# Performance work log

Hardware: AMD Instinct MI355X
Metric: run time of the kernel (lower is better)

Reference implementation:

```python
import jax, jax.numpy as jnp
import numpy as np

B, N, CS, CZ, H, CH, G, P = 2, 384, 384, 128, 8, 16, 2, 8
CZ4 = CZ // 4
INF = 1e5
UMAX = 3.0     # self.u_max
LMAX = 2.0     # self.log_scale_max
SQRT_CH = CH ** 0.5


def quat_to_rot(q):
    q = q / jnp.linalg.norm(q, axis=-1, keepdims=True)
    w, x, y, z = q[..., 0], q[..., 1], q[..., 2], q[..., 3]
    R = jnp.stack([
        1 - 2 * (y * y + z * z), 2 * (x * y - w * z), 2 * (x * z + w * y),
        2 * (x * y + w * z), 1 - 2 * (x * x + z * z), 2 * (y * z - w * x),
        2 * (x * z - w * y), 2 * (y * z + w * x), 1 - 2 * (x * x + y * y)], axis=-1)
    return R.reshape(q.shape[:-1] + (3, 3))


def robust_nll(delta, sigma):
    # inline robust 3x3 Cholesky solve: dist_sq = d^T S^-1 d, log_det = ln|S|
    eps = 1e-8
    s00 = sigma[..., 0, 0]; s01 = sigma[..., 0, 1]; s02 = sigma[..., 0, 2]
    s11 = sigma[..., 1, 1]; s12 = sigma[..., 1, 2]; s22 = sigma[..., 2, 2]
    d0 = delta[..., 0]; d1 = delta[..., 1]; d2 = delta[..., 2]
    l00_sq = jnp.maximum(s00, eps); inv_l00 = jax.lax.rsqrt(l00_sq)
    l10 = s01 * inv_l00; l20 = s02 * inv_l00
    l11_sq = jnp.maximum(s11 - l10 * l10, eps); inv_l11 = jax.lax.rsqrt(l11_sq)
    l21 = (s12 - l20 * l10) * inv_l11
    l22_sq = jnp.maximum(s22 - l20 * l20 - l21 * l21, eps); inv_l22 = jax.lax.rsqrt(l22_sq)
    log_det = jnp.log(l00_sq) + jnp.log(l11_sq) + jnp.log(l22_sq)
    y0 = d0 * inv_l00
    y1 = (d1 - l10 * y0) * inv_l11
    y2 = (d2 - l20 * y0 - l21 * y1) * inv_l22
    return y0 * y0 + y1 * y1 + y2 * y2, log_det


def iga_forward(s, z, mask, rot, trans, local_mean, scaling_log,
                Wq, Wk, Wv, Wb, bb, Wdz, bdz, Wqg, bqg, Wkg, bkg,
                Wvp, bvp, geo_scale, geo_bias, Wout, bout):
    # scalar q/k/v: [B,H,N,CH]
    q = (s @ Wq).reshape(B, N, H, CH).transpose(0, 2, 1, 3)
    k = (s @ Wk).reshape(B, N, H, CH).transpose(0, 2, 1, 3)
    v = (s @ Wv).reshape(B, N, H, CH).transpose(0, 2, 1, 3)
    logits = jnp.einsum('bhid,bhjd->bhij', q, k) / SQRT_CH
    # pair bias: [B,H,N,N]
    logits = logits + (z @ Wb + bb).transpose(0, 3, 1, 2)

    def parse(feat):  # -> u [B,N,H,G,3], s_log_delta [B,N,H,G,3]
        raw = feat.reshape(B, N, H, G, 6)
        return jnp.tanh(raw[..., :3]) * UMAX, jnp.tanh(raw[..., 3:]) * LMAX

    def to_global(u, sld):
        anchor = local_mean[:, :, None, None, :]
        base = scaling_log[:, :, None, None, :]
        sig_loc = jnp.maximum(jnp.exp(base + sld), 1e-6)
        pos = anchor + u * sig_loc
        mu = jnp.einsum('bnij,bnhgj->bnhgi', rot, pos) + trans[:, :, None, None, :]
        var = jnp.exp(2.0 * (base + sld))
        Sig = jnp.einsum('bnij,bnhgj,bnkj->bnhgik', rot, var, rot)  # R diag(var) R^T
        return mu.transpose(0, 2, 1, 3, 4), Sig.transpose(0, 2, 1, 3, 4, 5)

    qu, qs = parse(s @ Wqg + bqg)
    ku, ks = parse(s @ Wkg + bkg)
    q_mu, q_sig = to_global(qu, qs)   # [B,H,N,G,3], [B,H,N,G,3,3]
    k_mu, k_sig = to_global(ku, ks)
    delta = q_mu[:, :, :, None] - k_mu[:, :, None, :]      # [B,H,N,N,G,3]
    ssum = q_sig[:, :, :, None] + k_sig[:, :, None, :]     # [B,H,N,N,G,3,3]
    dist_sq, log_det = robust_nll(delta, ssum)
    geo = (-0.5 * dist_sq - 0.5 * log_det).sum(-1)          # [B,H,N,N]

    mask2d = mask[:, None, :, None] * mask[:, None, None, :]  # [B,1,N,N]
    a = jax.nn.softplus(geo_scale)[None, :, None, None]
    G_geo = a * (geo * mask2d) + geo_bias[None, :, None, None]
    logits = logits + G_geo + (1.0 - mask2d) * (-INF)
    w = jax.nn.softmax(logits, axis=-1)                      # [B,H,N,N]

    # scalar output
    o = jnp.einsum('bhij,bhjd->bihd', w, v).reshape(B, N, H * CH)
    # point output (IPA-style): to global, attend, back to local frame
    vpts = (s @ Wvp + bvp).reshape(B, N, H, P, 3)
    vpg = jnp.einsum('bnij,bnhpj->bnhpi', rot, vpts) + trans[:, :, None, None, :]
    vpg = vpg.transpose(0, 2, 1, 3, 4)                       # [B,H,N,P,3]
    opt = jnp.einsum('bhij,bhjpc->bhipc', w, vpg)            # [B,H,N,P,3]
    opt_local = jnp.einsum('bnji,bhnpj->bnhpi', rot, opt - trans[:, None, :, None, :])
    onorm = jnp.sqrt((opt_local ** 2).sum(-1) + 1e-8)        # [B,N,H,P]
    # pair output
    pz = z @ Wdz + bdz                                       # [B,N,N,CZ4]
    opair = jnp.einsum('bhij,bijc->bihc', w, pz)             # [B,N,H,CZ4]

    cat = jnp.concatenate([o, opt_local.reshape(B, N, H * P * 3),
                           onorm.reshape(B, N, H * P),
                           opair.reshape(B, N, H * CZ4)], axis=-1)  # [B,N,640]
    return cat @ Wout + bout


def setup_inputs() -> dict:
    ks = jax.random.split(jax.random.key(0), 24)
    rnd = lambda i, shape, sc=1.0: jax.random.normal(ks[i], shape, dtype=jnp.float32) * sc
    w = 0.02
    return dict(
        s=rnd(0, (B, N, CS)), z=rnd(1, (B, N, N, CZ)),
        mask=jnp.ones((B, N), jnp.float32),
        rot=quat_to_rot(rnd(2, (B, N, 4))),
        trans=rnd(3, (B, N, 3), 1.0),
        local_mean=rnd(4, (B, N, 3), 0.5),
        scaling_log=rnd(5, (B, N, 3), 0.1),
        Wq=rnd(6, (CS, H * CH), w), Wk=rnd(7, (CS, H * CH), w), Wv=rnd(8, (CS, H * CH), w),
        Wb=rnd(9, (CZ, H), w), bb=rnd(10, (H,), w),
        Wdz=rnd(11, (CZ, CZ4), w), bdz=rnd(12, (CZ4,), w),
        Wqg=rnd(13, (CS, H * G * 6), w), bqg=rnd(14, (H * G * 6,), w),
        Wkg=rnd(15, (CS, H * G * 6), w), bkg=rnd(16, (H * G * 6,), w),
        Wvp=rnd(17, (CS, H * P * 3), w), bvp=rnd(18, (H * P * 3,), w),
        geo_scale=jnp.ones((H,), jnp.float32), geo_bias=jnp.zeros((H,), jnp.float32),
        Wout=rnd(19, (H * (CH + P * 4 + CZ4), CS), w), bout=jnp.zeros((CS,), jnp.float32))


def reference(s, z, mask, rot, trans, local_mean, scaling_log, Wq, Wk, Wv, Wb, bb,
              Wdz, bdz, Wqg, bqg, Wkg, bkg, Wvp, bvp, geo_scale, geo_bias, Wout, bout):
    return iga_forward(s, z, mask, rot, trans, local_mean, scaling_log, Wq, Wk, Wv,
                       Wb, bb, Wdz, bdz, Wqg, bqg, Wkg, bkg, Wvp, bvp,
                       geo_scale, geo_bias, Wout, bout)
```

## Files before the change

kernel.cpp:

```cpp
#include <hip/hip_runtime.h>
#include <hip/hip_fp16.h>

#define NB   2
#define NN   384
#define NCS  384
#define NCZ  128
#define NH   8
#define NCH  16
#define NG   2
#define NP   8
#define NCZ4 32
#define BN   (NB*NN)
#define LINW 768

typedef _Float16 f16x8 __attribute__((ext_vector_type(8)));
typedef float    f32x4 __attribute__((ext_vector_type(4)));

__global__ void k_wprep(const float* __restrict__ Wb, const float* __restrict__ Wdz,
                        _Float16* __restrict__ wf) {
    int t = threadIdx.x;
    for (int e = t; e < 12*64*8; e += 256) {
        int r = e & 7, lane = (e >> 3) & 63, nk = e >> 9;
        int n = nk >> 2, kk = nk & 3;
        int c = kk*32 + (lane >> 4)*8 + r;
        int col = n*16 + (lane & 15);
        float w;
        if      (col < 8)  w = Wb[c*NH + col];
        else if (col < 40) w = Wdz[c*NCZ4 + (col-8)];
        else               w = 0.f;
        wf[e] = (_Float16)w;
    }
}

__global__ void k_rowlin(const float* __restrict__ s,
                         const float* __restrict__ Wq, const float* __restrict__ Wk,
                         const float* __restrict__ Wv,
                         const float* __restrict__ Wqg, const float* __restrict__ bqg,
                         const float* __restrict__ Wkg, const float* __restrict__ bkg,
                         const float* __restrict__ Wvp, const float* __restrict__ bvp,
                         float* __restrict__ lin,
                         float* __restrict__ kT, float* __restrict__ vT) {
    __shared__ float sl[4][NCS];
    int t  = threadIdx.x;
    int r0 = blockIdx.x * 4;
    for (int idx = t; idx < 4*NCS; idx += 256)
        sl[idx / NCS][idx % NCS] = s[(size_t)(r0 + idx/NCS)*NCS + (idx % NCS)];
    __syncthreads();
    int col = blockIdx.y * 256 + t;
    const float* W; int sw; float bias = 0.f;
    if      (col < 128) { W = Wq  + col;        sw = 128; }
    else if (col < 256) { W = Wk  + (col-128);  sw = 128; }
    else if (col < 384) { W = Wv  + (col-256);  sw = 128; }
    else if (col < 480) { W = Wqg + (col-384);  sw = 96;  bias = bqg[col-384]; }
    else if (col < 576) { W = Wkg + (col-480);  sw = 96;  bias = bkg[col-480]; }
    else                { W = Wvp + (col-576);  sw = 192; bias = bvp[col-576]; }
    float a0=0.f, a1=0.f, a2=0.f, a3=0.f;
    for (int c = 0; c < NCS; ++c) {
        float w = W[(size_t)c*sw];
        a0 = fmaf(sl[0][c], w, a0);
        a1 = fmaf(sl[1][c], w, a1);
        a2 = fmaf(sl[2][c], w, a2);
        a3 = fmaf(sl[3][c], w, a3);
    }
    lin[(size_t)(r0+0)*LINW + col] = a0 + bias;
    lin[(size_t)(r0+1)*LINW + col] = a1 + bias;
    lin[(size_t)(r0+2)*LINW + col] = a2 + bias;
    lin[(size_t)(r0+3)*LINW + col] = a3 + bias;
    if (col >= 128 && col < 384) {
        f32x4 v4; v4[0]=a0; v4[1]=a1; v4[2]=a2; v4[3]=a3;
        float* dst = (col < 256) ? (kT + (size_t)(col-128)*BN + r0)
                                 : (vT + (size_t)(col-256)*BN + r0);
        *(f32x4*)dst = v4;
    }
}

__global__ void k_geom(const float* __restrict__ lin, const float* __restrict__ rot,
                       const float* __restrict__ trans, const float* __restrict__ lm,
                       const float* __restrict__ sc,
                       float* __restrict__ qmu, float* __restrict__ qsig,
                       float* __restrict__ kmuT, float* __restrict__ ksigT,
                       float* __restrict__ vpgT) {
    int bn = blockIdx.x, t = threadIdx.x;
    __shared__ float R[9], T[3], A[3], Bs[3];
    if (t < 9) R[t] = rot[bn*9 + t];
    if (t < 3) { T[t] = trans[bn*3+t]; A[t] = lm[bn*3+t]; Bs[t] = sc[bn*3+t]; }
    __syncthreads();
    {
        int h = t >> 3, p = t & 7;
        const float* vr = lin + (size_t)bn*LINW + 576 + h*24 + p*3;
        float x = vr[0], y = vr[1], z = vr[2];
        int e = h*24 + p*3;
        vpgT[(size_t)(e+0)*BN + bn] = R[0]*x + R[1]*y + R[2]*z + T[0];
        vpgT[(size_t)(e+1)*BN + bn] = R[3]*x + R[4]*y + R[5]*z + T[1];
        vpgT[(size_t)(e+2)*BN + bn] = R[6]*x + R[7]*y + R[8]*z + T[2];
    }
    if (t < 32) {
        int side = t >> 4, item = t & 15;
        const float* raw = lin + (size_t)bn*LINW + (side ? 480 : 384) + item*6;
        float u0 = tanhf(raw[0])*3.f, u1 = tanhf(raw[1])*3.f, u2 = tanhf(raw[2])*3.f;
        float e0 = Bs[0] + tanhf(raw[3])*2.f;
        float e1 = Bs[1] + tanhf(raw[4])*2.f;
        float e2 = Bs[2] + tanhf(raw[5])*2.f;
        float sl0 = fmaxf(expf(e0), 1e-6f);
        float sl1 = fmaxf(expf(e1), 1e-6f);
        float sl2 = fmaxf(expf(e2), 1e-6f);
        float p0 = A[0] + u0*sl0, p1 = A[1] + u1*sl1, p2 = A[2] + u2*sl2;
        float mu0 = R[0]*p0 + R[1]*p1 + R[2]*p2 + T[0];
        float mu1 = R[3]*p0 + R[4]*p1 + R[5]*p2 + T[1];
        float mu2 = R[6]*p0 + R[7]*p1 + R[8]*p2 + T[2];
        float v0 = expf(2.f*e0), v1 = expf(2.f*e1), v2 = expf(2.f*e2);
        float s00 = R[0]*R[0]*v0 + R[1]*R[1]*v1 + R[2]*R[2]*v2;
        float s01 = R[0]*R[3]*v0 + R[1]*R[4]*v1 + R[2]*R[5]*v2;
        float s02 = R[0]*R[6]*v0 + R[1]*R[7]*v1 + R[2]*R[8]*v2;
        float s11 = R[3]*R[3]*v0 + R[4]*R[4]*v1 + R[5]*R[5]*v2;
        float s12 = R[3]*R[6]*v0 + R[4]*R[7]*v1 + R[5]*R[8]*v2;
        float s22 = R[6]*R[6]*v0 + R[7]*R[7]*v1 + R[8]*R[8]*v2;
        if (side) {
            kmuT[(size_t)(item*3+0)*BN + bn] = mu0;
            kmuT[(size_t)(item*3+1)*BN + bn] = mu1;
            kmuT[(size_t)(item*3+2)*BN + bn] = mu2;
            ksigT[(size_t)(item*6+0)*BN + bn] = s00;
            ksigT[(size_t)(item*6+1)*BN + bn] = s01;
            ksigT[(size_t)(item*6+2)*BN + bn] = s02;
            ksigT[(size_t)(item*6+3)*BN + bn] = s11;
            ksigT[(size_t)(item*6+4)*BN + bn] = s12;
            ksigT[(size_t)(item*6+5)*BN + bn] = s22;
        } else {
            float* mud = qmu + (size_t)bn*48 + item*3;
            mud[0]=mu0; mud[1]=mu1; mud[2]=mu2;
            float* sgd = qsig + (size_t)bn*96 + item*6;
            sgd[0]=s00; sgd[1]=s01; sgd[2]=s02; sgd[3]=s11; sgd[4]=s12; sgd[5]=s22;
        }
    }
}

__global__ void __launch_bounds__(256, 2)
k_attn(const float* __restrict__ z, const float* __restrict__ mask,
       const float* __restrict__ rot, const float* __restrict__ trans,
       const float* __restrict__ lin,
       const float* __restrict__ qmu, const float* __restrict__ qsig,
       const float* __restrict__ kmuT, const float* __restrict__ ksigT,
       const float* __restrict__ kT, const float* __restrict__ vT,
       const float* __restrict__ vpgT, const _Float16* __restrict__ wf,
       const float* __restrict__ bb, const float* __restrict__ bdz,
       const float* __restrict__ gsc, const float* __restrict__ gbi,
       float* __restrict__ cat) {
    __shared__ __align__(16) _Float16 zh[64*128];
    __shared__ float  logits[NH][NN];
    __shared__ __half pzl[NN][34];
    __shared__ float  qrow[128];
    __shared__ float  qmu_s[48], qsig_s[96];
    __shared__ float  Rm[9], Tv[3];
    __shared__ float  aH[NH], bH[NH];
    __shared__ float  bias_s[48];
    __shared__ float  maskI;

    int t  = threadIdx.x;
    int lane = t & 63, w = t >> 6;
    int b  = blockIdx.x / NN, i = blockIdx.x % NN;
    int bi = b*NN + i;
    const float* zbase = z + (size_t)bi*NN*NCZ;
    const size_t boff = (size_t)b*NN;

    const float* zrow0 = zbase + (size_t)(t >> 5)*NCZ + (t & 31)*4;
    float4 preA[8], preB[8];
    #pragma unroll
    for (int p = 0; p < 8; ++p) preA[p] = *(const float4*)(zrow0 + (size_t)(p*8)*NCZ);
    #pragma unroll
    for (int p = 0; p < 8; ++p) preB[p] = *(const float4*)(zrow0 + (size_t)(64 + p*8)*NCZ);

    if (t < 128) qrow[t] = lin[(size_t)bi*LINW + t];
    if (t < 48)  qmu_s[t] = qmu[(size_t)bi*48 + t];
    if (t < 48)  bias_s[t] = (t < 8) ? bb[t] : ((t < 40) ? bdz[t-8] : 0.f);
    if (t >= 64 && t < 160) qsig_s[t-64] = qsig[(size_t)bi*96 + (t-64)];
    if (t >= 160 && t < 169) Rm[t-160] = rot[bi*9 + (t-160)];
    if (t >= 169 && t < 172) Tv[t-169] = trans[bi*3 + (t-169)];
    if (t >= 176 && t < 184) {
        int h = t-176;
        float x = gsc[h];
        aH[h] = (x > 20.f) ? x : log1pf(expf(x));
        bH[h] = gbi[h];
    }
    if (t == 255) maskI = mask[bi];
    __syncthreads();

    {
        int h = t >> 5, lnn = t & 31;
        float qv[16];
        #pragma unroll
        for (int d = 0; d < 16; ++d) qv[d] = qrow[h*16 + d];
        float qm[6], qs[12];
        #pragma unroll
        for (int e = 0; e < 6; ++e)  qm[e] = qmu_s[h*6 + e];
        #pragma unroll
        for (int e = 0; e < 12; ++e) qs[e] = qsig_s[h*12 + e];
        float ascale = aH[h], hbias = bH[h], mI = maskI;
        #pragma unroll 1
        for (int jj = 0; jj < 3; ++jj) {
            int j4 = jj*128 + lnn*4;
            const float* kp = kT + (size_t)(h*16)*BN + boff + j4;
            f32x4 qk = {0.f,0.f,0.f,0.f};
            #pragma unroll
            for (int d = 0; d < 16; ++d) {
                f32x4 kv = *(const f32x4*)(kp + (size_t)d*BN);
                #pragma unroll
                for (int r = 0; r < 4; ++r) qk[r] = fmaf(qv[d], kv[r], qk[r]);
            }
            f32x4 geo = {0.f,0.f,0.f,0.f};
            #pragma unroll
            for (int g = 0; g < NG; ++g) {
                const float* kmb = kmuT + (size_t)((h*2+g)*3)*BN + boff + j4;
                f32x4 km0 = *(const f32x4*)(kmb);
                f32x4 km1 = *(const f32x4*)(kmb + BN);
                f32x4 km2 = *(const f32x4*)(kmb + 2*BN);
                const float* ksb = ksigT + (size_t)((h*2+g)*6)*BN + boff + j4;
                f32x4 ks0 = *(const f32x4*)(ksb);
                f32x4 ks1 = *(const f32x4*)(ksb + BN);
                f32x4 ks2 = *(const f32x4*)(ksb + 2*BN);
                f32x4 ks3 = *(const f32x4*)(ksb + 3*BN);
                f32x4 ks4 = *(const f32x4*)(ksb + 4*BN);
                f32x4 ks5 = *(const f32x4*)(ksb + 5*BN);
                #pragma unroll
                for (int r = 0; r < 4; ++r) {
                    float d0 = qm[g*3+0] - km0[r];
                    float d1 = qm[g*3+1] - km1[r];
                    float d2 = qm[g*3+2] - km2[r];
                    float s00 = qs[g*6+0] + ks0[r];
                    float s01 = qs[g*6+1] + ks1[r];
                    float s02 = qs[g*6+2] + ks2[r];
                    float s11 = qs[g*6+3] + ks3[r];
                    float s12 = qs[g*6+4] + ks4[r];
                    float s22 = qs[g*6+5] + ks5[r];
                    float l00 = fmaxf(s00, 1e-8f);
                    float i00 = rsqrtf(l00);
                    float l10 = s01*i00, l20 = s02*i00;
                    float l11 = fmaxf(s11 - l10*l10, 1e-8f);
                    float i11 = rsqrtf(l11);
                    float l21 = (s12 - l20*l10)*i11;
                    float l22 = fmaxf(s22 - l20*l20 - l21*l21, 1e-8f);
                    float i22 = rsqrtf(l22);
                    float ld = __logf(l00) + __logf(l11) + __logf(l22);
                    float y0 = d0*i00;
                    float y1 = (d1 - l10*y0)*i11;
                    float y2 = (d2 - l20*y0 - l21*y1)*i22;
                    geo[r] += -0.5f*(y0*y0 + y1*y1 + y2*y2 + ld);
                }
            }
            f32x4 mv = *(const f32x4*)(mask + boff + j4);
            f32x4 lg;
            #pragma unroll
            for (int r = 0; r < 4; ++r) {
                float m2 = mI * mv[r];
                lg[r] = qk[r]*0.25f + ascale*(geo[r]*m2) + hbias + (1.f - m2)*(-100000.f);
            }
            *(f32x4*)&logits[h][j4] = lg;
        }
    }

    f16x8 bfr[12];
    #pragma unroll
    for (int nk = 0; nk < 12; ++nk)
        bfr[nk] = ((const f16x8*)wf)[nk*64 + lane];

    int srow0 = t >> 5;
    int scb   = (t & 31) * 8;
    int sswz  = (srow0 & 7) << 4;
    int arow  = w*16 + (lane & 15);
    int abase = arow*256 + ((lane >> 4) << 4);
    int akey  = (lane & 7) << 4;
    int ccol  = lane & 15;
    int cjl   = w*16 + (lane >> 4)*4;

#define CHUNK_BODY(CH, PRE)                                                          \
    {                                                                                \
        _Pragma("unroll")                                                            \
        for (int p = 0; p < 8; ++p) {                                                \
            union { _Float16 h[4]; unsigned long long u; } pk;                       \
            pk.h[0] = (_Float16)PRE[p].x; pk.h[1] = (_Float16)PRE[p].y;              \
            pk.h[2] = (_Float16)PRE[p].z; pk.h[3] = (_Float16)PRE[p].w;              \
            *(unsigned long long*)((char*)zh + (p*8 + srow0)*256 + (scb ^ sswz)) = pk.u; \
        }                                                                            \
        if ((CH) + 2 < 6) {                                                          \
            const float* src = zbase + (size_t)((CH+2)*64)*NCZ + (size_t)(t>>5)*NCZ  \
                               + (t & 31)*4;                                         \
            _Pragma("unroll")                                                        \
            for (int p = 0; p < 8; ++p)                                              \
                PRE[p] = *(const float4*)(src + (size_t)(p*8)*NCZ);                  \
        }                                                                            \
        __syncthreads();                                                             \
        {                                                                            \
            f16x8 af0 = *(const f16x8*)((const char*)zh + ((abase +   0) ^ akey));   \
            f16x8 af1 = *(const f16x8*)((const char*)zh + ((abase +  64) ^ akey));   \
            f16x8 af2 = *(const f16x8*)((const char*)zh + ((abase + 128) ^ akey));   \
            f16x8 af3 = *(const f16x8*)((const char*)zh + ((abase + 192) ^ akey));   \
            f32x4 ac0 = {0.f,0.f,0.f,0.f}, ac1 = ac0, ac2 = ac0;                     \
            ac0 = __builtin_amdgcn_mfma_f32_16x16x32_f16(af0, bfr[0], ac0, 0,0,0);   \
            ac1 = __builtin_amdgcn_mfma_f32_16x16x32_f16(af0, bfr[4], ac1, 0,0,0);   \
            ac2 = __builtin_amdgcn_mfma_f32_16x16x32_f16(af0, bfr[8], ac2, 0,0,0);   \
            ac0 = __builtin_amdgcn_mfma_f32_16x16x32_f16(af1, bfr[1], ac0, 0,0,0);   \
            ac1 = __builtin_amdgcn_mfma_f32_16x16x32_f16(af1, bfr[5], ac1, 0,0,0);   \
            ac2 = __builtin_amdgcn_mfma_f32_16x16x32_f16(af1, bfr[9], ac2, 0,0,0);   \
            ac0 = __builtin_amdgcn_mfma_f32_16x16x32_f16(af2, bfr[2], ac0, 0,0,0);   \
            ac1 = __builtin_amdgcn_mfma_f32_16x16x32_f16(af2, bfr[6], ac1, 0,0,0);   \
            ac2 = __builtin_amdgcn_mfma_f32_16x16x32_f16(af2, bfr[10], ac2, 0,0,0);  \
            ac0 = __builtin_amdgcn_mfma_f32_16x16x32_f16(af3, bfr[3], ac0, 0,0,0);   \
            ac1 = __builtin_amdgcn_mfma_f32_16x16x32_f16(af3, bfr[7], ac1, 0,0,0);   \
            ac2 = __builtin_amdgcn_mfma_f32_16x16x32_f16(af3, bfr[11], ac2, 0,0,0);  \
            int jg = (CH)*64 + cjl;                                                  \
            _Pragma("unroll")                                                        \
            for (int r = 0; r < 4; ++r) {                                            \
                int j = jg + r;                                                      \
                float v0 = ac0[r] + bias_s[ccol];                                    \
                if (ccol < 8) logits[ccol][j] += v0;                                 \
                else          pzl[j][ccol-8] = __float2half(v0);                     \
                pzl[j][ccol+8] = __float2half(ac1[r] + bias_s[16+ccol]);             \
                if (ccol < 8)                                                        \
                    pzl[j][ccol+24] = __float2half(ac2[r] + bias_s[32+ccol]);        \
            }                                                                        \
        }                                                                            \
        __syncthreads();                                                             \
    }

    CHUNK_BODY(0, preA)
    CHUNK_BODY(1, preB)
    CHUNK_BODY(2, preA)
    CHUNK_BODY(3, preB)
    CHUNK_BODY(4, preA)
    CHUNK_BODY(5, preB)
#undef CHUNK_BODY

    int h = t >> 5, lnn = t & 31;
    float mx = -3.4e38f;
    #pragma unroll
    for (int jj = 0; jj < 12; ++jj) mx = fmaxf(mx, logits[h][lnn + jj*32]);
    #pragma unroll
    for (int m = 16; m >= 1; m >>= 1) mx = fmaxf(mx, __shfl_xor(mx, m, 64));
    float se = 0.f;
    #pragma unroll
    for (int jj = 0; jj < 12; ++jj) {
        int j = lnn + jj*32;
        float e = __expf(logits[h][j] - mx);
        logits[h][j] = e;
        se += e;
    }
    #pragma unroll
    for (int m = 16; m >= 1; m >>= 1) se += __shfl_xor(se, m, 64);
    float inv = 1.f / se;

    float o[16], op[24], opa[32];
    #pragma unroll
    for (int d = 0; d < 16; ++d) o[d] = 0.f;
    #pragma unroll
    for (int e = 0; e < 24; ++e) op[e] = 0.f;
    #pragma unroll
    for (int c = 0; c < 32; ++c) opa[c] = 0.f;

    const float* vbase = vT + (size_t)(h*16)*BN + boff + lnn;
    const float* gbase = vpgT + (size_t)(h*24)*BN + boff + lnn;
    #pragma unroll 1
    for (int jj = 0; jj < 12; ++jj) {
        int j = lnn + jj*32;
        float wgt = logits[h][j] * inv;
        const float* vb = vbase + jj*32;
        #pragma unroll
        for (int d = 0; d < 16; ++d) o[d] = fmaf(wgt, vb[(size_t)d*BN], o[d]);
        const float* gb = gbase + jj*32;
        #pragma unroll
        for (int e = 0; e < 24; ++e) op[e] = fmaf(wgt, gb[(size_t)e*BN], op[e]);
        const __half2* pzp = reinterpret_cast<const __half2*>(&pzl[j][0]);
        #pragma unroll
        for (int c2 = 0; c2 < 16; ++c2) {
            float2 pf = __half22float2(pzp[c2]);
            opa[2*c2]   = fmaf(wgt, pf.x, opa[2*c2]);
            opa[2*c2+1] = fmaf(wgt, pf.y, opa[2*c2+1]);
        }
    }
    #pragma unroll
    for (int m = 16; m >= 1; m >>= 1) {
        #pragma unroll
        for (int d = 0; d < 16; ++d) o[d] += __shfl_xor(o[d], m, 64);
        #pragma unroll
        for (int e = 0; e < 24; ++e) op[e] += __shfl_xor(op[e], m, 64);
        #pragma unroll
        for (int c = 0; c < 32; ++c) opa[c] += __shfl_xor(opa[c], m, 64);
    }
    if (lnn == 0) {
        float* cp = cat + (size_t)bi*640;
        #pragma unroll
        for (int d = 0; d < 16; ++d) cp[h*16 + d] = o[d];
        #pragma unroll
        for (int p = 0; p < 8; ++p) {
            float x  = op[p*3+0] - Tv[0];
            float y  = op[p*3+1] - Tv[1];
            float zz = op[p*3+2] - Tv[2];
            float l0 = Rm[0]*x + Rm[3]*y + Rm[6]*zz;
            float l1 = Rm[1]*x + Rm[4]*y + Rm[7]*zz;
            float l2 = Rm[2]*x + Rm[5]*y + Rm[8]*zz;
            cp[128 + h*24 + p*3 + 0] = l0;
            cp[128 + h*24 + p*3 + 1] = l1;
            cp[128 + h*24 + p*3 + 2] = l2;
            cp[320 + h*8 + p] = sqrtf(l0*l0 + l1*l1 + l2*l2 + 1e-8f);
        }
        #pragma unroll
        for (int c = 0; c < 32; ++c) cp[384 + h*32 + c] = opa[c];
    }
}

__global__ void k_out(const float* __restrict__ cat, const float* __restrict__ Wout,
                      const float* __restrict__ bout, float* __restrict__ out) {
    __shared__ float cl[4][640];
    int t  = threadIdx.x;
    int r0 = blockIdx.x * 4;
    for (int idx = t; idx < 4*640; idx += 384)
        cl[idx/640][idx%640] = cat[(size_t)(r0 + idx/640)*640 + (idx%640)];
    __syncthreads();
    int col = t;
    float a0=0.f, a1=0.f, a2=0.f, a3=0.f;
    for (int c = 0; c < 640; ++c) {
        float w = Wout[(size_t)c*NCS + col];
        a0 = fmaf(cl[0][c], w, a0);
        a1 = fmaf(cl[1][c], w, a1);
        a2 = fmaf(cl[2][c], w, a2);
        a3 = fmaf(cl[3][c], w, a3);
    }
    float bv = bout[col];
    out[(size_t)(r0+0)*NCS + col] = a0 + bv;
    out[(size_t)(r0+1)*NCS + col] = a1 + bv;
    out[(size_t)(r0+2)*NCS + col] = a2 + bv;
    out[(size_t)(r0+3)*NCS + col] = a3 + bv;
}

extern "C" void kernel_launch(void* const* d_in, const int* in_sizes, int n_in,
                              void* d_out, int out_size, void* d_ws, size_t ws_size,
                              hipStream_t stream) {
    const float* s    = (const float*)d_in[0];
    const float* z    = (const float*)d_in[1];
    const float* mask = (const float*)d_in[2];
    const float* rot  = (const float*)d_in[3];
    const float* trans= (const float*)d_in[4];
    const float* lm   = (const float*)d_in[5];
    const float* sc   = (const float*)d_in[6];
    const float* Wq   = (const float*)d_in[7];
    const float* Wk   = (const float*)d_in[8];
    const float* Wv   = (const float*)d_in[9];
    const float* Wb   = (const float*)d_in[10];
    const float* bb   = (const float*)d_in[11];
    const float* Wdz  = (const float*)d_in[12];
    const float* bdz  = (const float*)d_in[13];
    const float* Wqg  = (const float*)d_in[14];
    const float* bqg  = (const float*)d_in[15];
    const float* Wkg  = (const float*)d_in[16];
    const float* bkg  = (const float*)d_in[17];
    const float* Wvp  = (const float*)d_in[18];
    const float* bvp  = (const float*)d_in[19];
    const float* gsc  = (const float*)d_in[20];
    const float* gbi  = (const float*)d_in[21];
    const float* Wout = (const float*)d_in[22];
    const float* bout = (const float*)d_in[23];
    float* out = (float*)d_out;

    float* ws    = (float*)d_ws;
    float* lin   = ws;
    float* qmu   = lin   + 589824;
    float* qsig  = qmu   + 36864;
    float* kmuT  = qsig  + 73728;
    float* ksigT = kmuT  + 36864;
    float* vpgT  = ksigT + 73728;
    float* kT    = vpgT  + 147456;
    float* vT    = kT    + 98304;
    float* cat   = vT    + 98304;
    _Float16* wf = (_Float16*)(cat + 491520);

    k_wprep<<<1, 256, 0, stream>>>(Wb, Wdz, wf);
    k_rowlin<<<dim3(192, 3), 256, 0, stream>>>(s, Wq, Wk, Wv, Wqg, bqg, Wkg, bkg,
                                               Wvp, bvp, lin, kT, vT);
    k_geom<<<BN, 64, 0, stream>>>(lin, rot, trans, lm, sc, qmu, qsig, kmuT, ksigT, vpgT);
    k_attn<<<BN, 256, 0, stream>>>(z, mask, rot, trans, lin, qmu, qsig, kmuT, ksigT,
                                   kT, vT, vpgT, wf, bb, bdz, gsc, gbi, cat);
    k_out<<<192, 384, 0, stream>>>(cat, Wout, bout, out);
}
```

Baseline: 158.5 us.

## Split pair-feature projection of z into its own high-parallelism kernel

Moves the MFMA projection of z (pair bias plus down-projected pair features) out of the attention kernel into a separate kernel launched over BN*6 blocks. That kernel writes the bias to a global fp32 buffer and the pair features to a global fp16 buffer, which the attention kernel then reads. The aim is to stream the large z tensor with more blocks and better occupancy, and to shrink the attention kernel's shared memory so it can run at higher occupancy. The cost is an extra round trip of intermediates through global memory and one more kernel launch.

```diff
diff --git a/kernel.cpp b/kernel.cpp
--- a/kernel.cpp
+++ b/kernel.cpp
@@ -12,6 +12,7 @@
 #define NCZ4 32
 #define BN   (NB*NN)
 #define LINW 768
+#define PZW  40
 
 typedef _Float16 f16x8 __attribute__((ext_vector_type(8)));
 typedef float    f32x4 __attribute__((ext_vector_type(4)));
@@ -29,6 +30,90 @@
         else if (col < 40) w = Wdz[c*NCZ4 + (col-8)];
         else               w = 0.f;
         wf[e] = (_Float16)w;
+    }
+}
+
+__global__ void __launch_bounds__(256, 4)
+k_zproj(const float* __restrict__ z, const _Float16* __restrict__ wf,
+        const float* __restrict__ bb, const float* __restrict__ bdz,
+        float* __restrict__ zbg, __half* __restrict__ pzg) {
+    __shared__ __align__(16) _Float16 zh[64*128];
+    __shared__ float  zbT[8][64];
+    __shared__ __align__(16) __half pzt[64][PZW];
+    __shared__ float  bias_s[48];
+
+    int t = threadIdx.x;
+    int lane = t & 63, w = t >> 6;
+    int bi = blockIdx.x / 6, ch = blockIdx.x % 6;
+    const float* zbase = z + ((size_t)bi*NN + ch*64)*NCZ;
+
+    const float* src = zbase + (size_t)(t >> 5)*NCZ + (t & 31)*4;
+    float4 pre[8];
+    #pragma unroll
+    for (int p = 0; p < 8; ++p) pre[p] = *(const float4*)(src + (size_t)(p*8)*NCZ);
+
+    f16x8 bfr[12];
+    #pragma unroll
+    for (int nk = 0; nk < 12; ++nk)
+        bfr[nk] = ((const f16x8*)wf)[nk*64 + lane];
+    if (t < 48) bias_s[t] = (t < 8) ? bb[t] : ((t < 40) ? bdz[t-8] : 0.f);
+
+    int srow0 = t >> 5;
+    int scb   = (t & 31) * 8;
+    int sswz  = (srow0 & 7) << 4;
+    #pragma unroll
+    for (int p = 0; p < 8; ++p) {
+        union { _Float16 h[4]; unsigned long long u; } pk;
+        pk.h[0] = (_Float16)pre[p].x; pk.h[1] = (_Float16)pre[p].y;
+        pk.h[2] = (_Float16)pre[p].z; pk.h[3] = (_Float16)pre[p].w;
+        *(unsigned long long*)((char*)zh + (p*8 + srow0)*256 + (scb ^ sswz)) = pk.u;
+    }
+    __syncthreads();
+
+    int arow  = w*16 + (lane & 15);
+    int abase = arow*256 + ((lane >> 4) << 4);
+    int akey  = (lane & 7) << 4;
+    int ccol  = lane & 15;
+    int cjl   = w*16 + (lane >> 4)*4;
+    f16x8 af0 = *(const f16x8*)((const char*)zh + ((abase +   0) ^ akey));
+    f16x8 af1 = *(const f16x8*)((const char*)zh + ((abase +  64) ^ akey));
+    f16x8 af2 = *(const f16x8*)((const char*)zh + ((abase + 128) ^ akey));
+    f16x8 af3 = *(const f16x8*)((const char*)zh + ((abase + 192) ^ akey));
+    f32x4 ac0 = {0.f,0.f,0.f,0.f}, ac1 = ac0, ac2 = ac0;
+    ac0 = __builtin_amdgcn_mfma_f32_16x16x32_f16(af0, bfr[0], ac0, 0,0,0);
+    ac1 = __builtin_amdgcn_mfma_f32_16x16x32_f16(af0, bfr[4], ac1, 0,0,0);
+    ac2 = __builtin_amdgcn_mfma_f32_16x16x32_f16(af0, bfr[8], ac2, 0,0,0);
+    ac0 = __builtin_amdgcn_mfma_f32_16x16x32_f16(af1, bfr[1], ac0, 0,0,0);
+    ac1 = __builtin_amdgcn_mfma_f32_16x16x32_f16(af1, bfr[5], ac1, 0,0,0);
+    ac2 = __builtin_amdgcn_mfma_f32_16x16x32_f16(af1, bfr[9], ac2, 0,0,0);
+    ac0 = __builtin_amdgcn_mfma_f32_16x16x32_f16(af2, bfr[2], ac0, 0,0,0);
+    ac1 = __builtin_amdgcn_mfma_f32_16x16x32_f16(af2, bfr[6], ac1, 0,0,0);
+    ac2 = __builtin_amdgcn_mfma_f32_16x16x32_f16(af2, bfr[10], ac2, 0,0,0);
+    ac0 = __builtin_amdgcn_mfma_f32_16x16x32_f16(af3, bfr[3], ac0, 0,0,0);
+    ac1 = __builtin_amdgcn_mfma_f32_16x16x32_f16(af3, bfr[7], ac1, 0,0,0);
+    ac2 = __builtin_amdgcn_mfma_f32_16x16x32_f16(af3, bfr[11], ac2, 0,0,0);
+    #pragma unroll
+    for (int r = 0; r < 4; ++r) {
+        int j = cjl + r;
+        float v0 = ac0[r] + bias_s[ccol];
+        if (ccol < 8) zbT[ccol][j] = v0;
+        else          pzt[j][ccol-8] = __float2half(v0);
+        pzt[j][ccol+8] = __float2half(ac1[r] + bias_s[16+ccol]);
+        if (ccol < 8)
+            pzt[j][ccol+24] = __float2half(ac2[r] + bias_s[32+ccol]);
+    }
+    __syncthreads();
+
+    {
+        int e = t*2, h = e >> 6, j = e & 63;
+        float2 v; v.x = zbT[h][j]; v.y = zbT[h][j+1];
+        *(float2*)(zbg + ((size_t)bi*NH + h)*NN + ch*64 + j) = v;
+    }
+    {
+        const uint4* sp = (const uint4*)pzt;
+        uint4* dp = (uint4*)(pzg + ((size_t)bi*NN + ch*64)*PZW);
+        dp[t] = sp[t];
+        if (t < 64) dp[256 + t] = sp[256 + t];
     }
 }
 
@@ -134,44 +219,31 @@
     }
 }
 
-__global__ void __launch_bounds__(256, 2)
-k_attn(const float* __restrict__ z, const float* __restrict__ mask,
-       const float* __restrict__ rot, const float* __restrict__ trans,
-       const float* __restrict__ lin,
-       const float* __restrict__ qmu, const float* __restrict__ qsig,
-       const float* __restrict__ kmuT, const float* __restrict__ ksigT,
-       const float* __restrict__ kT, const float* __restrict__ vT,
-       const float* __restrict__ vpgT, const _Float16* __restrict__ wf,
-       const float* __restrict__ bb, const float* __restrict__ bdz,
-       const float* __restrict__ gsc, const float* __restrict__ gbi,
-       float* __restrict__ cat) {
-    __shared__ __align__(16) _Float16 zh[64*128];
+__global__ void __launch_bounds__(256, 4)
+k_attn2(const float* __restrict__ mask,
+        const float* __restrict__ rot, const float* __restrict__ trans,
+        const float* __restrict__ lin,
+        const float* __restrict__ qmu, const float* __restrict__ qsig,
+        const float* __restrict__ kmuT, const float* __restrict__ ksigT,
+        const float* __restrict__ kT, const float* __restrict__ vT,
+        const float* __restrict__ vpgT,
+        const float* __restrict__ zbg, const __half* __restrict__ pzg,
+        const float* __restrict__ gsc, const float* __restrict__ gbi,
+        float* __restrict__ cat) {
     __shared__ float  logits[NH][NN];
-    __shared__ __half pzl[NN][34];
     __shared__ float  qrow[128];
     __shared__ float  qmu_s[48], qsig_s[96];
     __shared__ float  Rm[9], Tv[3];
     __shared__ float  aH[NH], bH[NH];
-    __shared__ float  bias_s[48];
     __shared__ float  maskI;
 
     int t  = threadIdx.x;
-    int lane = t & 63, w = t >> 6;
     int b  = blockIdx.x / NN, i = blockIdx.x % NN;
     int bi = b*NN + i;
-    const float* zbase = z + (size_t)bi*NN*NCZ;
     const size_t boff = (size_t)b*NN;
-
-    const float* zrow0 = zbase + (size_t)(t >> 5)*NCZ + (t & 31)*4;
-    float4 preA[8], preB[8];
-    #pragma unroll
-    for (int p = 0; p < 8; ++p) preA[p] = *(const float4*)(zrow0 + (size_t)(p*8)*NCZ);
-    #pragma unroll
-    for (int p = 0; p < 8; ++p) preB[p] = *(const float4*)(zrow0 + (size_t)(64 + p*8)*NCZ);
 
     if (t < 128) qrow[t] = lin[(size_t)bi*LINW + t];
     if (t < 48)  qmu_s[t] = qmu[(size_t)bi*48 + t];
-    if (t < 48)  bias_s[t] = (t < 8) ? bb[t] : ((t < 40) ? bdz[t-8] : 0.f);
     if (t >= 64 && t < 160) qsig_s[t-64] = qsig[(size_t)bi*96 + (t-64)];
     if (t >= 160 && t < 169) Rm[t-160] = rot[bi*9 + (t-160)];
     if (t >= 169 && t < 172) Tv[t-169] = trans[bi*3 + (t-169)];
@@ -184,8 +256,8 @@
     if (t == 255) maskI = mask[bi];
     __syncthreads();
 
+    int h = t >> 5, lnn = t & 31;
     {
-        int h = t >> 5, lnn = t & 31;
         float qv[16];
         #pragma unroll
         for (int d = 0; d < 16; ++d) qv[d] = qrow[h*16 + d];
@@ -246,90 +318,20 @@
                     geo[r] += -0.5f*(y0*y0 + y1*y1 + y2*y2 + ld);
                 }
             }
-            f32x4 mv = *(const f32x4*)(mask + boff + j4);
+            f32x4 zb4 = *(const f32x4*)(zbg + ((size_t)bi*NH + h)*NN + j4);
+            f32x4 mv  = *(const f32x4*)(mask + boff + j4);
             f32x4 lg;
             #pragma unroll
             for (int r = 0; r < 4; ++r) {
                 float m2 = mI * mv[r];
-                lg[r] = qk[r]*0.25f + ascale*(geo[r]*m2) + hbias + (1.f - m2)*(-100000.f);
+                lg[r] = qk[r]*0.25f + zb4[r] + ascale*(geo[r]*m2) + hbias
+                        + (1.f - m2)*(-100000.f);
             }
             *(f32x4*)&logits[h][j4] = lg;
         }
     }
-
-    f16x8 bfr[12];
-    #pragma unroll
-    for (int nk = 0; nk < 12; ++nk)
-        bfr[nk] = ((const f16x8*)wf)[nk*64 + lane];
-
-    int srow0 = t >> 5;
-    int scb   = (t & 31) * 8;
-    int sswz  = (srow0 & 7) << 4;
-    int arow  = w*16 + (lane & 15);
-    int abase = arow*256 + ((lane >> 4) << 4);
-    int akey  = (lane & 7) << 4;
-    int ccol  = lane & 15;
-    int cjl   = w*16 + (lane >> 4)*4;
-
-#define CHUNK_BODY(CH, PRE)                                                          \
-    {                                                                                \
-        _Pragma("unroll")                                                            \
-        for (int p = 0; p < 8; ++p) {                                                \
-            union { _Float16 h[4]; unsigned long long u; } pk;                       \
-            pk.h[0] = (_Float16)PRE[p].x; pk.h[1] = (_Float16)PRE[p].y;              \
-            pk.h[2] = (_Float16)PRE[p].z; pk.h[3] = (_Float16)PRE[p].w;              \
-            *(unsigned long long*)((char*)zh + (p*8 + srow0)*256 + (scb ^ sswz)) = pk.u; \
-        }                                                                            \
-        if ((CH) + 2 < 6) {                                                          \
-            const float* src = zbase + (size_t)((CH+2)*64)*NCZ + (size_t)(t>>5)*NCZ  \
-                               + (t & 31)*4;                                         \
-            _Pragma("unroll")                                                        \
-            for (int p = 0; p < 8; ++p)                                              \
-                PRE[p] = *(const float4*)(src + (size_t)(p*8)*NCZ);                  \
-        }                                                                            \
-        __syncthreads();                                                             \
-        {                                                                            \
-            f16x8 af0 = *(const f16x8*)((const char*)zh + ((abase +   0) ^ akey));   \
-            f16x8 af1 = *(const f16x8*)((const char*)zh + ((abase +  64) ^ akey));   \
-            f16x8 af2 = *(const f16x8*)((const char*)zh + ((abase + 128) ^ akey));   \
-            f16x8 af3 = *(const f16x8*)((const char*)zh + ((abase + 192) ^ akey));   \
-            f32x4 ac0 = {0.f,0.f,0.f,0.f}, ac1 = ac0, ac2 = ac0;                     \
-            ac0 = __builtin_amdgcn_mfma_f32_16x16x32_f16(af0, bfr[0], ac0, 0,0,0);   \
-            ac1 = __builtin_amdgcn_mfma_f32_16x16x32_f16(af0, bfr[4], ac1, 0,0,0);   \
-            ac2 = __builtin_amdgcn_mfma_f32_16x16x32_f16(af0, bfr[8], ac2, 0,0,0);   \
-            ac0 = __builtin_amdgcn_mfma_f32_16x16x32_f16(af1, bfr[1], ac0, 0,0,0);   \
-            ac1 = __builtin_amdgcn_mfma_f32_16x16x32_f16(af1, bfr[5], ac1, 0,0,0);   \
-            ac2 = __builtin_amdgcn_mfma_f32_16x16x32_f16(af1, bfr[9], ac2, 0,0,0);   \
-            ac0 = __builtin_amdgcn_mfma_f32_16x16x32_f16(af2, bfr[2], ac0, 0,0,0);   \
-            ac1 = __builtin_amdgcn_mfma_f32_16x16x32_f16(af2, bfr[6], ac1, 0,0,0);   \
-            ac2 = __builtin_amdgcn_mfma_f32_16x16x32_f16(af2, bfr[10], ac2, 0,0,0);  \
-            ac0 = __builtin_amdgcn_mfma_f32_16x16x32_f16(af3, bfr[3], ac0, 0,0,0);   \
-            ac1 = __builtin_amdgcn_mfma_f32_16x16x32_f16(af3, bfr[7], ac1, 0,0,0);   \
-            ac2 = __builtin_amdgcn_mfma_f32_16x16x32_f16(af3, bfr[11], ac2, 0,0,0);  \
-            int jg = (CH)*64 + cjl;                                                  \
-            _Pragma("unroll")                                                        \
-            for (int r = 0; r < 4; ++r) {                                            \
-                int j = jg + r;                                                      \
-                float v0 = ac0[r] + bias_s[ccol];                                    \
-                if (ccol < 8) logits[ccol][j] += v0;                                 \
-                else          pzl[j][ccol-8] = __float2half(v0);                     \
-                pzl[j][ccol+8] = __float2half(ac1[r] + bias_s[16+ccol]);             \
-                if (ccol < 8)                                                        \
-                    pzl[j][ccol+24] = __float2half(ac2[r] + bias_s[32+ccol]);        \
-            }                                                                        \
-        }                                                                            \
-        __syncthreads();                                                             \
-    }
-
-    CHUNK_BODY(0, preA)
-    CHUNK_BODY(1, preB)
-    CHUNK_BODY(2, preA)
-    CHUNK_BODY(3, preB)
-    CHUNK_BODY(4, preA)
-    CHUNK_BODY(5, preB)
-#undef CHUNK_BODY
-
-    int h = t >> 5, lnn = t & 31;
+    __syncthreads();
+
     float mx = -3.4e38f;
     #pragma unroll
     for (int jj = 0; jj < 12; ++jj) mx = fmaxf(mx, logits[h][lnn + jj*32]);
@@ -367,7 +369,7 @@
         const float* gb = gbase + jj*32;
         #pragma unroll
         for (int e = 0; e < 24; ++e) op[e] = fmaf(wgt, gb[(size_t)e*BN], op[e]);
-        const __half2* pzp = reinterpret_cast<const __half2*>(&pzl[j][0]);
+        const __half2* pzp = (const __half2*)(pzg + ((size_t)bi*NN + j)*PZW);
         #pragma unroll
         for (int c2 = 0; c2 < 16; ++c2) {
             float2 pf = __half22float2(pzp[c2]);
@@ -469,13 +471,16 @@
     float* kT    = vpgT  + 147456;
     float* vT    = kT    + 98304;
     float* cat   = vT    + 98304;
-    _Float16* wf = (_Float16*)(cat + 491520);
+    float* zbg   = cat   + 491520;
+    _Float16* wf = (_Float16*)(zbg + 2359296);
+    __half* pzg  = (__half*)((float*)wf + 3072);
 
     k_wprep<<<1, 256, 0, stream>>>(Wb, Wdz, wf);
+    k_zproj<<<BN*6, 256, 0, stream>>>(z, wf, bb, bdz, zbg, pzg);
     k_rowlin<<<dim3(192, 3), 256, 0, stream>>>(s, Wq, Wk, Wv, Wqg, bqg, Wkg, bkg,
                                                Wvp, bvp, lin, kT, vT);
     k_geom<<<BN, 64, 0, stream>>>(lin, rot, trans, lm, sc, qmu, qsig, kmuT, ksigT, vpgT);
-    k_attn<<<BN, 256, 0, stream>>>(z, mask, rot, trans, lin, qmu, qsig, kmuT, ksigT,
-                                   kT, vT, vpgT, wf, bb, bdz, gsc, gbi, cat);
+    k_attn2<<<BN, 256, 0, stream>>>(mask, rot, trans, lin, qmu, qsig, kmuT, ksigT,
+                                    kT, vT, vpgT, zbg, pzg, gsc, gbi, cat);
     k_out<<<192, 384, 0, stream>>>(cat, Wout, bout, out);
 }
```

After: 229.6 us. 1.45x slower.
